# Kernel optimization log

Hardware: AMD Instinct MI355X
Metric: run time of the kernel (lower is better)

Reference implementation:

```python
import jax, jax.numpy as jnp
import numpy as np

IN_FEATURES = 512
HIDDEN = 512


def setup_inputs() -> dict:
    key = jax.random.key(0)
    ks = jax.random.split(key, 7)
    s = 1.0 / np.sqrt(IN_FEATURES)
    return {
        "x": jax.random.normal(ks[0], (8, 2048, IN_FEATURES), dtype=jnp.float32),
        "Wq": jax.random.uniform(ks[1], (IN_FEATURES, HIDDEN), jnp.float32, -s, s),
        "bq": jax.random.uniform(ks[2], (HIDDEN,), jnp.float32, -s, s),
        "Wk": jax.random.uniform(ks[3], (IN_FEATURES, HIDDEN), jnp.float32, -s, s),
        "bk": jax.random.uniform(ks[4], (HIDDEN,), jnp.float32, -s, s),
        "Wv": jax.random.uniform(ks[5], (IN_FEATURES, HIDDEN), jnp.float32, -s, s),
        "bv": jax.random.uniform(ks[6], (HIDDEN,), jnp.float32, -s, s),
    }


def reference(x, Wq, bq, Wk, bk, Wv, bv):
    # q,k,v: [b, s, h]
    q = jnp.einsum("bsf,fh->bsh", x, Wq) + bq
    k = jnp.einsum("bsf,fh->bsh", x, Wk) + bk
    v = jnp.einsum("bsf,fh->bsh", x, Wv) + bv
    # NOTE: no 1/sqrt(d) scaling, matching the original module.
    scores = jnp.einsum("bqh,bkh->bqk", q, k)  # [b, s, s]
    attn = jax.nn.softmax(scores, axis=-1)
    return jnp.einsum("bqk,bkh->bqh", attn, v)
```

## Files before the change

kernel.cpp:

```cpp
#include <hip/hip_runtime.h>
#include <hip/hip_fp16.h>


typedef _Float16 f16;
typedef __attribute__((ext_vector_type(8))) _Float16 f16x8;
typedef __attribute__((ext_vector_type(4))) _Float16 f16x4;
typedef __attribute__((ext_vector_type(4))) float f32x4;
typedef __attribute__((address_space(3))) char lds_t;

#define GADDR(p) ((const __attribute__((address_space(1))) void*)(p))
#define LADDR(p) ((__attribute__((address_space(3))) void*)(p))

__device__ __forceinline__ unsigned lds_u32(void* p) {
    return (unsigned)(unsigned long long)(lds_t*)p;
}

#define DSRD(dst, a) asm volatile("ds_read_b128 %0, %1" : "=v"(dst) : "v"(a))
#define WAITV0 asm volatile("s_waitcnt vmcnt(0)" ::: "memory")
#define WAITV4 asm volatile("s_waitcnt vmcnt(4)" ::: "memory")
#define WAITV8 asm volatile("s_waitcnt vmcnt(8)" ::: "memory")
#define WAITLG0 asm volatile("s_waitcnt lgkmcnt(0)" ::: "memory")

__device__ __forceinline__ void xcd_remap(int& bx, int& by, int& bz) {
    const int gx = gridDim.x, gy = gridDim.y;
    const int nwg = gx * gy * gridDim.z;
    const int f = (blockIdx.z * gy + blockIdx.y) * gx + blockIdx.x;
    int L = (f & 7) * (nwg >> 3) + (f >> 3);
    bx = L % gx; int r = L / gx; by = r % gy; bz = r / gy;
}

__global__ __launch_bounds__(256) void k_cvt(const float* __restrict__ x,
                                             f16* __restrict__ xh,
                                             const float* __restrict__ Wq,
                                             const float* __restrict__ Wk,
                                             const float* __restrict__ Wv,
                                             f16* __restrict__ Wt) {
    int bid = blockIdx.x;
    if (bid < 8192) {
        long i = (long)bid * 256 + threadIdx.x;
        float4 v = ((const float4*)x)[i];
        f16x4 h = { (f16)v.x, (f16)v.y, (f16)v.z, (f16)v.w };
        ((f16x4*)xh)[i] = h;
    } else {
        int id = (bid - 8192) * 256 + threadIdx.x;
        int w = id >> 18, rem = id & 262143;
        int kk = rem >> 9, n = rem & 511;
        const float* W = (w == 0) ? Wq : (w == 1) ? Wk : Wv;
        Wt[((long)w << 18) + ((long)n << 9) + kk] = (f16)W[((long)kk << 9) + n];
    }
}

#define G128STAGE(BUF, K0)                                                                  \
  { _Pragma("unroll") for (int i_ = 0; i_ < 4; ++i_) {                                      \
      const f16* sa_ = A + (rowA0 + i_ * 32 + (tid >> 3)) * (long)K + (K0) + colSw;         \
      __builtin_amdgcn_global_load_lds(GADDR(sa_),                                          \
          LADDR(smem + (BUF) * 32768 + i_ * 4096 + wave * 1024), 16, 0, 0);                 \
      const f16* sb_ = Bt + (rowB0 + i_ * 32 + (tid >> 3)) * (long)K + (K0) + colSw;        \
      __builtin_amdgcn_global_load_lds(GADDR(sb_),                                          \
          LADDR(smem + (BUF) * 32768 + 16384 + i_ * 4096 + wave * 1024), 16, 0, 0);         \
    } }

template <int MODE, int NT>
__global__ __launch_bounds__(256) void k_g128(const f16* __restrict__ Ain,
                                              const f16* __restrict__ Btin,
                                              void* __restrict__ Cv,
                                              void* __restrict__ CvAlt,
                                              const float* __restrict__ b0,
                                              const float* __restrict__ b1,
                                              const float* __restrict__ b2,
                                              int N,
                                              long sA, long sB, long sC) {
    constexpr int K = NT << 6;

    int bxi, byi, bz;
    xcd_remap(bxi, byi, bz);
    const f16* A  = Ain  + bz * sA;
    const f16* Bt = Btin + bz * sB;
    __shared__ __align__(16) char smem[65536];
    const unsigned sbase = lds_u32(smem);

    const int tid = threadIdx.x;
    const int wave = tid >> 6, lane = tid & 63;
    const int l15 = lane & 15, l4 = lane >> 4;
    const int wm = (wave >> 1) * 64, wn = (wave & 1) * 64;
    const long rowA0 = (long)byi * 128;
    const long rowB0 = (long)bxi * 128;

    const unsigned sw = (unsigned)((l15 & 7) << 4);
    const unsigned cb0 = (unsigned)(l4 * 16) ^ sw;
    const unsigned cb1 = (unsigned)(64 + l4 * 16) ^ sw;
    const int colSw = (((tid & 7) ^ ((tid >> 3) & 7)) << 3);

    f32x4 acc[4][4] = {};

    G128STAGE(0, 0);
    int cur = 0;
#pragma unroll 1
    for (int t = 0; t < NT; ++t) {
        if (t + 1 < NT) { G128STAGE(cur ^ 1, (t + 1) << 6); WAITV8; }
        else            { WAITV0; }
        __builtin_amdgcn_s_barrier();

        f16x8 af[4][2], bf[4][2];
        const unsigned aB = sbase + (unsigned)cur * 32768u;
        const unsigned bB = aB + 16384u;
#pragma unroll
        for (int mi = 0; mi < 4; ++mi) {
            unsigned ra = wm + mi * 16 + l15;
            DSRD(af[mi][0], aB + ra * 128 + cb0);
            DSRD(af[mi][1], aB + ra * 128 + cb1);
        }
#pragma unroll
        for (int nj = 0; nj < 4; ++nj) {
            unsigned rb = wn + nj * 16 + l15;
            DSRD(bf[nj][0], bB + rb * 128 + cb0);
            DSRD(bf[nj][1], bB + rb * 128 + cb1);
        }
        WAITLG0;
        __builtin_amdgcn_sched_barrier(0);
        __builtin_amdgcn_s_setprio(1);
#pragma unroll
        for (int mi = 0; mi < 4; ++mi)
#pragma unroll
            for (int nj = 0; nj < 4; ++nj)
#pragma unroll
                for (int ks = 0; ks < 2; ++ks)
                    acc[mi][nj] = __builtin_amdgcn_mfma_f32_16x16x32_f16(
                        af[mi][ks], bf[nj][ks], acc[mi][nj], 0, 0, 0);
        __builtin_amdgcn_s_setprio(0);
        __builtin_amdgcn_s_barrier();
        cur ^= 1;
    }

    if constexpr (MODE == 0) {
        float* C = (float*)Cv + bz * sC;
#pragma unroll
        for (int mi = 0; mi < 4; ++mi)
#pragma unroll
            for (int nj = 0; nj < 4; ++nj) {
                long gr = rowA0 + wm + mi * 16 + l4 * 4;
                int  gc = (int)rowB0 + wn + nj * 16 + l15;
#pragma unroll
                for (int r = 0; r < 4; ++r)
                    C[(gr + r) * (long)N + gc] = acc[mi][nj][r];
            }
    } else {
        if (bz == 2) {
            f16* VT = (f16*)CvAlt;
#pragma unroll
            for (int mi = 0; mi < 4; ++mi)
#pragma unroll
                for (int nj = 0; nj < 4; ++nj) {
                    long gr = rowA0 + wm + mi * 16 + l4 * 4;
                    int  gc = (int)rowB0 + wn + nj * 16 + l15;
                    float bv_ = b2[gc];
                    long b = gr >> 11, sL = gr & 2047;
                    f16x4 o = { (f16)(acc[mi][nj][0] + bv_),
                                (f16)(acc[mi][nj][1] + bv_),
                                (f16)(acc[mi][nj][2] + bv_),
                                (f16)(acc[mi][nj][3] + bv_) };
                    *(f16x4*)(VT + (b << 20) + ((long)gc << 11) + sL) = o;
                }
        } else {
            const float* bias = (bz == 0) ? b0 : b1;
            f16* C = (f16*)Cv + bz * sC;
#pragma unroll
            for (int mi = 0; mi < 4; ++mi)
#pragma unroll
                for (int nj = 0; nj < 4; ++nj) {
                    long gr = rowA0 + wm + mi * 16 + l4 * 4;
                    int  gc = (int)rowB0 + wn + nj * 16 + l15;
                    float bv_ = bias[gc];
#pragma unroll
                    for (int r = 0; r < 4; ++r)
                        C[(gr + r) * (long)N + gc] = (f16)(acc[mi][nj][r] + bv_);
                }
        }
    }
}

#define S512STAGE(BUF, K0)                                                                  \
  { _Pragma("unroll") for (int i_ = 0; i_ < 2; ++i_) {                                      \
      const f16* sa_ = A + (rowA0 + i_ * 64 + (tid >> 3)) * 512L + (K0) + colSw;            \
      __builtin_amdgcn_global_load_lds(GADDR(sa_),                                          \
          LADDR(smem + (BUF) * 32768 + i_ * 8192 + wid * 1024), 16, 0, 0);                  \
      const f16* sb_ = Bt + (rowB0 + i_ * 64 + (tid >> 3)) * 512L + (K0) + colSw;           \
      __builtin_amdgcn_global_load_lds(GADDR(sb_),                                          \
          LADDR(smem + (BUF) * 32768 + 16384 + i_ * 8192 + wid * 1024), 16, 0, 0);          \
    } }

__global__ __launch_bounds__(512) void k_scores512(const f16* __restrict__ Ain,
                                                   const f16* __restrict__ Btin,
                                                   f16* __restrict__ Cv) {
    constexpr int NT = 8;
    int bxi, byi, bz;
    xcd_remap(bxi, byi, bz);
    const f16* A  = Ain  + (long)bz * 2048 * 512;
    const f16* Bt = Btin + (long)bz * 2048 * 512;
    __shared__ __align__(16) char smem[65536];
    const unsigned sbase = lds_u32(smem);

    const int tid = threadIdx.x;
    const int wid = tid >> 6, lane = tid & 63;
    const int l15 = lane & 15, l4 = lane >> 4;
    const int wm = (wid >> 2) * 64, wn = (wid & 3) * 32;
    const long rowA0 = (long)byi * 128;
    const long rowB0 = (long)bxi * 128;

    const unsigned sw = (unsigned)((l15 & 7) << 4);
    const unsigned cb0 = (unsigned)(l4 * 16) ^ sw;
    const unsigned cb1 = (unsigned)(64 + l4 * 16) ^ sw;
    const int colSw = (((tid & 7) ^ ((tid >> 3) & 7)) << 3);

    f32x4 acc[4][2] = {};

    S512STAGE(0, 0);
    int cur = 0;
#pragma unroll 1
    for (int t = 0; t < NT; ++t) {
        if (t + 1 < NT) { S512STAGE(cur ^ 1, (t + 1) << 6); WAITV4; }
        else            { WAITV0; }
        __builtin_amdgcn_s_barrier();

        f16x8 af[4][2], bf[2][2];
        const unsigned aB = sbase + (unsigned)cur * 32768u;
        const unsigned bB = aB + 16384u;
#pragma unroll
        for (int mi = 0; mi < 4; ++mi) {
            unsigned ra = wm + mi * 16 + l15;
            DSRD(af[mi][0], aB + ra * 128 + cb0);
            DSRD(af[mi][1], aB + ra * 128 + cb1);
        }
#pragma unroll
        for (int nj = 0; nj < 2; ++nj) {
            unsigned rb = wn + nj * 16 + l15;
            DSRD(bf[nj][0], bB + rb * 128 + cb0);
            DSRD(bf[nj][1], bB + rb * 128 + cb1);
        }
        WAITLG0;
        __builtin_amdgcn_sched_barrier(0);
        __builtin_amdgcn_s_setprio(1);
#pragma unroll
        for (int mi = 0; mi < 4; ++mi)
#pragma unroll
            for (int nj = 0; nj < 2; ++nj)
#pragma unroll
                for (int ks = 0; ks < 2; ++ks)
                    acc[mi][nj] = __builtin_amdgcn_mfma_f32_16x16x32_f16(
                        af[mi][ks], bf[nj][ks], acc[mi][nj], 0, 0, 0);
        __builtin_amdgcn_s_setprio(0);
        __builtin_amdgcn_s_barrier();
        cur ^= 1;
    }

    f16* C = Cv + (long)bz * 2048 * 2048;
#pragma unroll
    for (int mi = 0; mi < 4; ++mi)
#pragma unroll
        for (int nj = 0; nj < 2; ++nj) {
            long gr = rowA0 + wm + mi * 16 + l4 * 4;
            int  gc = (int)rowB0 + wn + nj * 16 + l15;
#pragma unroll
            for (int r = 0; r < 4; ++r)
                C[(gr + r) * 2048L + gc] = (f16)acc[mi][nj][r];
        }
}

__global__ __launch_bounds__(256) void k_softmax(f16* __restrict__ P) {
    const long row = blockIdx.x;
    f16* p = P + row * 2048;
    const int tid = threadIdx.x, lane = tid & 63, wave = tid >> 6;

    f16x8 v = ((const f16x8*)p)[tid];
    float f[8];
#pragma unroll
    for (int j = 0; j < 8; ++j) f[j] = (float)v[j];
    float m = fmaxf(fmaxf(fmaxf(f[0], f[1]), fmaxf(f[2], f[3])),
                    fmaxf(fmaxf(f[4], f[5]), fmaxf(f[6], f[7])));
#pragma unroll
    for (int off = 32; off; off >>= 1) m = fmaxf(m, __shfl_xor(m, off));

    __shared__ float red[4];
    __shared__ float bc[2];
    if (lane == 0) red[wave] = m;
    __syncthreads();
    if (tid == 0) bc[0] = fmaxf(fmaxf(red[0], red[1]), fmaxf(red[2], red[3]));
    __syncthreads();
    m = bc[0];

    float e[8], sum = 0.f;
#pragma unroll
    for (int j = 0; j < 8; ++j) { e[j] = __expf(f[j] - m); sum += e[j]; }
#pragma unroll
    for (int off = 32; off; off >>= 1) sum += __shfl_xor(sum, off);
    if (lane == 0) red[wave] = sum;
    __syncthreads();
    if (tid == 0) bc[1] = (red[0] + red[1]) + (red[2] + red[3]);
    __syncthreads();
    float inv = 1.f / bc[1];

    f16x8 o;
#pragma unroll
    for (int j = 0; j < 8; ++j) o[j] = (f16)(e[j] * inv);
    ((f16x8*)p)[tid] = o;
}

extern "C" void kernel_launch(void* const* d_in, const int* in_sizes, int n_in,
                              void* d_out, int out_size, void* d_ws, size_t ws_size,
                              hipStream_t stream) {
    const float* x  = (const float*)d_in[0];
    const float* Wq = (const float*)d_in[1];
    const float* bq = (const float*)d_in[2];
    const float* Wk = (const float*)d_in[3];
    const float* bk = (const float*)d_in[4];
    const float* Wv = (const float*)d_in[5];
    const float* bv = (const float*)d_in[6];
    float* out = (float*)d_out;

    char* ws = (char*)d_ws;
    f16* vt = (f16*)(ws + 0);
    f16* xh = (f16*)(ws + 33554432);
    f16* Wt = (f16*)(ws + 50331648);
    f16* P8 = (f16*)(ws + 33554432);
    f16* qh = (f16*)d_out;
    f16* kh = (f16*)((char*)d_out + 16777216);

    k_cvt<<<11264, 256, 0, stream>>>(x, xh, Wq, Wk, Wv, Wt);

    k_g128<1, 8><<<dim3(4, 128, 3), 256, 0, stream>>>(
        xh, Wt, qh, vt, bq, bk, bv, 512,
        0, (long)512 * 512, (long)16384 * 512);

    k_scores512<<<dim3(16, 16, 8), 512, 0, stream>>>(qh, kh, P8);

    k_softmax<<<16384, 256, 0, stream>>>(P8);

    k_g128<0, 32><<<dim3(4, 16, 8), 256, 0, stream>>>(
        P8, vt, out, nullptr, nullptr, nullptr, nullptr, 512,
        (long)2048 * 2048, (long)512 * 2048, (long)2048 * 512);
}
```

Baseline: 154.2 us.

## Use K=32 tiles with half the LDS for projection and scores GEMMs

```diff
diff --git a/kernel.cpp b/kernel.cpp
--- a/kernel.cpp
+++ b/kernel.cpp
@@ -50,33 +50,34 @@
     }
 }
 
-#define G128STAGE(BUF, K0)                                                                  \
-  { _Pragma("unroll") for (int i_ = 0; i_ < 4; ++i_) {                                      \
-      const f16* sa_ = A + (rowA0 + i_ * 32 + (tid >> 3)) * (long)K + (K0) + colSw;         \
+
+#define B32STAGE(BUF, K0)                                                                   \
+  { _Pragma("unroll") for (int i_ = 0; i_ < 2; ++i_) {                                      \
+      const f16* sa_ = A + (rowA0 + i_ * 64 + (tid >> 2)) * (long)K + (K0) + colSw;         \
       __builtin_amdgcn_global_load_lds(GADDR(sa_),                                          \
-          LADDR(smem + (BUF) * 32768 + i_ * 4096 + wave * 1024), 16, 0, 0);                 \
-      const f16* sb_ = Bt + (rowB0 + i_ * 32 + (tid >> 3)) * (long)K + (K0) + colSw;        \
+          LADDR(smem + (BUF) * 16384 + i_ * 4096 + wave * 1024), 16, 0, 0);                 \
+      const f16* sb_ = Bt + (rowB0 + i_ * 64 + (tid >> 2)) * (long)K + (K0) + colSw;        \
       __builtin_amdgcn_global_load_lds(GADDR(sb_),                                          \
-          LADDR(smem + (BUF) * 32768 + 16384 + i_ * 4096 + wave * 1024), 16, 0, 0);         \
+          LADDR(smem + (BUF) * 16384 + 8192 + i_ * 4096 + wave * 1024), 16, 0, 0);          \
     } }
 
 template <int MODE, int NT>
-__global__ __launch_bounds__(256) void k_g128(const f16* __restrict__ Ain,
-                                              const f16* __restrict__ Btin,
-                                              void* __restrict__ Cv,
-                                              void* __restrict__ CvAlt,
-                                              const float* __restrict__ b0,
-                                              const float* __restrict__ b1,
-                                              const float* __restrict__ b2,
-                                              int N,
-                                              long sA, long sB, long sC) {
-    constexpr int K = NT << 6;
+__global__ __launch_bounds__(256) void k_b32(const f16* __restrict__ Ain,
+                                             const f16* __restrict__ Btin,
+                                             void* __restrict__ Cv,
+                                             void* __restrict__ CvAlt,
+                                             const float* __restrict__ b0,
+                                             const float* __restrict__ b1,
+                                             const float* __restrict__ b2,
+                                             int N,
+                                             long sA, long sB, long sC) {
+    constexpr int K = NT << 5;
 
     int bxi, byi, bz;
     xcd_remap(bxi, byi, bz);
     const f16* A  = Ain  + bz * sA;
     const f16* Bt = Btin + bz * sB;
-    __shared__ __align__(16) char smem[65536];
+    __shared__ __align__(16) char smem[32768];
     const unsigned sbase = lds_u32(smem);
 
     const int tid = threadIdx.x;
@@ -86,36 +87,29 @@
     const long rowA0 = (long)byi * 128;
     const long rowB0 = (long)bxi * 128;
 
-    const unsigned sw = (unsigned)((l15 & 7) << 4);
-    const unsigned cb0 = (unsigned)(l4 * 16) ^ sw;
-    const unsigned cb1 = (unsigned)(64 + l4 * 16) ^ sw;
-    const int colSw = (((tid & 7) ^ ((tid >> 3) & 7)) << 3);
+    const unsigned sw = (unsigned)(((l15 & 3) ^ ((l15 >> 2) & 3)) << 4);
+    const unsigned cb = (unsigned)(l4 * 16) ^ sw;
+    const int colSw = (((tid & 3) ^ ((tid >> 2) & 3) ^ ((tid >> 4) & 3)) << 3);
 
     f32x4 acc[4][4] = {};
 
-    G128STAGE(0, 0);
+    B32STAGE(0, 0);
     int cur = 0;
 #pragma unroll 1
     for (int t = 0; t < NT; ++t) {
-        if (t + 1 < NT) { G128STAGE(cur ^ 1, (t + 1) << 6); WAITV8; }
+        if (t + 1 < NT) { B32STAGE(cur ^ 1, (t + 1) << 5); WAITV4; }
         else            { WAITV0; }
         __builtin_amdgcn_s_barrier();
 
-        f16x8 af[4][2], bf[4][2];
-        const unsigned aB = sbase + (unsigned)cur * 32768u;
-        const unsigned bB = aB + 16384u;
-#pragma unroll
-        for (int mi = 0; mi < 4; ++mi) {
-            unsigned ra = wm + mi * 16 + l15;
-            DSRD(af[mi][0], aB + ra * 128 + cb0);
-            DSRD(af[mi][1], aB + ra * 128 + cb1);
-        }
-#pragma unroll
-        for (int nj = 0; nj < 4; ++nj) {
-            unsigned rb = wn + nj * 16 + l15;
-            DSRD(bf[nj][0], bB + rb * 128 + cb0);
-            DSRD(bf[nj][1], bB + rb * 128 + cb1);
-        }
+        f16x8 af[4], bf[4];
+        const unsigned aB = sbase + (unsigned)cur * 16384u;
+        const unsigned bB = aB + 8192u;
+#pragma unroll
+        for (int mi = 0; mi < 4; ++mi)
+            DSRD(af[mi], aB + (wm + mi * 16 + l15) * 64 + cb);
+#pragma unroll
+        for (int nj = 0; nj < 4; ++nj)
+            DSRD(bf[nj], bB + (wn + nj * 16 + l15) * 64 + cb);
         WAITLG0;
         __builtin_amdgcn_sched_barrier(0);
         __builtin_amdgcn_s_setprio(1);
@@ -123,28 +117,14 @@
         for (int mi = 0; mi < 4; ++mi)
 #pragma unroll
             for (int nj = 0; nj < 4; ++nj)
-#pragma unroll
-                for (int ks = 0; ks < 2; ++ks)
-                    acc[mi][nj] = __builtin_amdgcn_mfma_f32_16x16x32_f16(
-                        af[mi][ks], bf[nj][ks], acc[mi][nj], 0, 0, 0);
+                acc[mi][nj] = __builtin_amdgcn_mfma_f32_16x16x32_f16(
+                    af[mi], bf[nj], acc[mi][nj], 0, 0, 0);
         __builtin_amdgcn_s_setprio(0);
         __builtin_amdgcn_s_barrier();
         cur ^= 1;
     }
 
-    if constexpr (MODE == 0) {
-        float* C = (float*)Cv + bz * sC;
-#pragma unroll
-        for (int mi = 0; mi < 4; ++mi)
-#pragma unroll
-            for (int nj = 0; nj < 4; ++nj) {
-                long gr = rowA0 + wm + mi * 16 + l4 * 4;
-                int  gc = (int)rowB0 + wn + nj * 16 + l15;
-#pragma unroll
-                for (int r = 0; r < 4; ++r)
-                    C[(gr + r) * (long)N + gc] = acc[mi][nj][r];
-            }
-    } else {
+    if constexpr (MODE == 1) {
         if (bz == 2) {
             f16* VT = (f16*)CvAlt;
 #pragma unroll
@@ -176,34 +156,49 @@
                         C[(gr + r) * (long)N + gc] = (f16)(acc[mi][nj][r] + bv_);
                 }
         }
+    } else {
+        f16* C = (f16*)Cv + bz * sC;
+#pragma unroll
+        for (int mi = 0; mi < 4; ++mi)
+#pragma unroll
+            for (int nj = 0; nj < 4; ++nj) {
+                long gr = rowA0 + wm + mi * 16 + l4 * 4;
+                int  gc = (int)rowB0 + wn + nj * 16 + l15;
+#pragma unroll
+                for (int r = 0; r < 4; ++r)
+                    C[(gr + r) * (long)N + gc] = (f16)acc[mi][nj][r];
+            }
     }
 }
 
-#define S512STAGE(BUF, K0)                                                                  \
-  { _Pragma("unroll") for (int i_ = 0; i_ < 2; ++i_) {                                      \
-      const f16* sa_ = A + (rowA0 + i_ * 64 + (tid >> 3)) * 512L + (K0) + colSw;            \
+#define G128STAGE(BUF, K0)                                                                  \
+  { _Pragma("unroll") for (int i_ = 0; i_ < 4; ++i_) {                                      \
+      const f16* sa_ = A + (rowA0 + i_ * 32 + (tid >> 3)) * (long)K + (K0) + colSw;         \
       __builtin_amdgcn_global_load_lds(GADDR(sa_),                                          \
-          LADDR(smem + (BUF) * 32768 + i_ * 8192 + wid * 1024), 16, 0, 0);                  \
-      const f16* sb_ = Bt + (rowB0 + i_ * 64 + (tid >> 3)) * 512L + (K0) + colSw;           \
+          LADDR(smem + (BUF) * 32768 + i_ * 4096 + wave * 1024), 16, 0, 0);                 \
+      const f16* sb_ = Bt + (rowB0 + i_ * 32 + (tid >> 3)) * (long)K + (K0) + colSw;        \
       __builtin_amdgcn_global_load_lds(GADDR(sb_),                                          \
-          LADDR(smem + (BUF) * 32768 + 16384 + i_ * 8192 + wid * 1024), 16, 0, 0);          \
+          LADDR(smem + (BUF) * 32768 + 16384 + i_ * 4096 + wave * 1024), 16, 0, 0);         \
     } }
 
-__global__ __launch_bounds__(512) void k_scores512(const f16* __restrict__ Ain,
-                                                   const f16* __restrict__ Btin,
-                                                   f16* __restrict__ Cv) {
-    constexpr int NT = 8;
+template <int NT>
+__global__ __launch_bounds__(256) void k_g128(const f16* __restrict__ Ain,
+                                              const f16* __restrict__ Btin,
+                                              float* __restrict__ Cout,
+                                              int N, long sA, long sB, long sC) {
+    constexpr int K = NT << 6;
+
     int bxi, byi, bz;
     xcd_remap(bxi, byi, bz);
-    const f16* A  = Ain  + (long)bz * 2048 * 512;
-    const f16* Bt = Btin + (long)bz * 2048 * 512;
+    const f16* A  = Ain  + bz * sA;
+    const f16* Bt = Btin + bz * sB;
     __shared__ __align__(16) char smem[65536];
     const unsigned sbase = lds_u32(smem);
 
     const int tid = threadIdx.x;
-    const int wid = tid >> 6, lane = tid & 63;
+    const int wave = tid >> 6, lane = tid & 63;
     const int l15 = lane & 15, l4 = lane >> 4;
-    const int wm = (wid >> 2) * 64, wn = (wid & 3) * 32;
+    const int wm = (wave >> 1) * 64, wn = (wave & 1) * 64;
     const long rowA0 = (long)byi * 128;
     const long rowB0 = (long)bxi * 128;
 
@@ -212,17 +207,17 @@
     const unsigned cb1 = (unsigned)(64 + l4 * 16) ^ sw;
     const int colSw = (((tid & 7) ^ ((tid >> 3) & 7)) << 3);
 
-    f32x4 acc[4][2] = {};
-
-    S512STAGE(0, 0);
+    f32x4 acc[4][4] = {};
+
+    G128STAGE(0, 0);
     int cur = 0;
 #pragma unroll 1
     for (int t = 0; t < NT; ++t) {
-        if (t + 1 < NT) { S512STAGE(cur ^ 1, (t + 1) << 6); WAITV4; }
+        if (t + 1 < NT) { G128STAGE(cur ^ 1, (t + 1) << 6); WAITV8; }
         else            { WAITV0; }
         __builtin_amdgcn_s_barrier();
 
-        f16x8 af[4][2], bf[2][2];
+        f16x8 af[4][2], bf[4][2];
         const unsigned aB = sbase + (unsigned)cur * 32768u;
         const unsigned bB = aB + 16384u;
 #pragma unroll
@@ -232,7 +227,7 @@
             DSRD(af[mi][1], aB + ra * 128 + cb1);
         }
 #pragma unroll
-        for (int nj = 0; nj < 2; ++nj) {
+        for (int nj = 0; nj < 4; ++nj) {
             unsigned rb = wn + nj * 16 + l15;
             DSRD(bf[nj][0], bB + rb * 128 + cb0);
             DSRD(bf[nj][1], bB + rb * 128 + cb1);
@@ -243,7 +238,7 @@
 #pragma unroll
         for (int mi = 0; mi < 4; ++mi)
 #pragma unroll
-            for (int nj = 0; nj < 2; ++nj)
+            for (int nj = 0; nj < 4; ++nj)
 #pragma unroll
                 for (int ks = 0; ks < 2; ++ks)
                     acc[mi][nj] = __builtin_amdgcn_mfma_f32_16x16x32_f16(
@@ -253,16 +248,16 @@
         cur ^= 1;
     }
 
-    f16* C = Cv + (long)bz * 2048 * 2048;
+    float* C = Cout + bz * sC;
 #pragma unroll
     for (int mi = 0; mi < 4; ++mi)
 #pragma unroll
-        for (int nj = 0; nj < 2; ++nj) {
+        for (int nj = 0; nj < 4; ++nj) {
             long gr = rowA0 + wm + mi * 16 + l4 * 4;
             int  gc = (int)rowB0 + wn + nj * 16 + l15;
 #pragma unroll
             for (int r = 0; r < 4; ++r)
-                C[(gr + r) * 2048L + gc] = (f16)acc[mi][nj][r];
+                C[(gr + r) * (long)N + gc] = acc[mi][nj][r];
         }
 }
 
@@ -327,15 +322,17 @@
 
     k_cvt<<<11264, 256, 0, stream>>>(x, xh, Wq, Wk, Wv, Wt);
 
-    k_g128<1, 8><<<dim3(4, 128, 3), 256, 0, stream>>>(
+    k_b32<1, 16><<<dim3(4, 128, 3), 256, 0, stream>>>(
         xh, Wt, qh, vt, bq, bk, bv, 512,
         0, (long)512 * 512, (long)16384 * 512);
 
-    k_scores512<<<dim3(16, 16, 8), 512, 0, stream>>>(qh, kh, P8);
+    k_b32<2, 16><<<dim3(16, 16, 8), 256, 0, stream>>>(
+        qh, kh, P8, nullptr, nullptr, nullptr, nullptr, 2048,
+        (long)2048 * 512, (long)2048 * 512, (long)2048 * 2048);
 
     k_softmax<<<16384, 256, 0, stream>>>(P8);
 
-    k_g128<0, 32><<<dim3(4, 16, 8), 256, 0, stream>>>(
-        P8, vt, out, nullptr, nullptr, nullptr, nullptr, 512,
+    k_g128<32><<<dim3(4, 16, 8), 256, 0, stream>>>(
+        P8, vt, out, 512,
         (long)2048 * 2048, (long)512 * 2048, (long)2048 * 512);
 }
```

After: 162.8 us. 1.06x slower.

## Chain four column tiles per scores block to overlap epilogue stores with loads

Applied to the files above, without the earlier changes.

```diff
diff --git a/kernel.cpp b/kernel.cpp
--- a/kernel.cpp
+++ b/kernel.cpp
@@ -19,6 +19,7 @@
 #define WAITV0 asm volatile("s_waitcnt vmcnt(0)" ::: "memory")
 #define WAITV4 asm volatile("s_waitcnt vmcnt(4)" ::: "memory")
 #define WAITV8 asm volatile("s_waitcnt vmcnt(8)" ::: "memory")
+#define WAITV36 asm volatile("s_waitcnt vmcnt(36)" ::: "memory")
 #define WAITLG0 asm volatile("s_waitcnt lgkmcnt(0)" ::: "memory")
 
 __device__ __forceinline__ void xcd_remap(int& bx, int& by, int& bz) {
@@ -179,12 +180,12 @@
     }
 }
 
-#define S512STAGE(BUF, K0)                                                                  \
+#define S512STAGE(BUF, RB, K0)                                                              \
   { _Pragma("unroll") for (int i_ = 0; i_ < 2; ++i_) {                                      \
       const f16* sa_ = A + (rowA0 + i_ * 64 + (tid >> 3)) * 512L + (K0) + colSw;            \
       __builtin_amdgcn_global_load_lds(GADDR(sa_),                                          \
           LADDR(smem + (BUF) * 32768 + i_ * 8192 + wid * 1024), 16, 0, 0);                  \
-      const f16* sb_ = Bt + (rowB0 + i_ * 64 + (tid >> 3)) * 512L + (K0) + colSw;           \
+      const f16* sb_ = Bt + ((RB) + i_ * 64 + (tid >> 3)) * 512L + (K0) + colSw;            \
       __builtin_amdgcn_global_load_lds(GADDR(sb_),                                          \
           LADDR(smem + (BUF) * 32768 + 16384 + i_ * 8192 + wid * 1024), 16, 0, 0);          \
     } }
@@ -192,7 +193,6 @@
 __global__ __launch_bounds__(512) void k_scores512(const f16* __restrict__ Ain,
                                                    const f16* __restrict__ Btin,
                                                    f16* __restrict__ Cv) {
-    constexpr int NT = 8;
     int bxi, byi, bz;
     xcd_remap(bxi, byi, bz);
     const f16* A  = Ain  + (long)bz * 2048 * 512;
@@ -205,21 +205,28 @@
     const int l15 = lane & 15, l4 = lane >> 4;
     const int wm = (wid >> 2) * 64, wn = (wid & 3) * 32;
     const long rowA0 = (long)byi * 128;
-    const long rowB0 = (long)bxi * 128;
+    const long chain0 = (long)bxi * 4;
 
     const unsigned sw = (unsigned)((l15 & 7) << 4);
     const unsigned cb0 = (unsigned)(l4 * 16) ^ sw;
     const unsigned cb1 = (unsigned)(64 + l4 * 16) ^ sw;
     const int colSw = (((tid & 7) ^ ((tid >> 3) & 7)) << 3);
 
+    f16* C = Cv + (long)bz * 2048 * 2048;
     f32x4 acc[4][2] = {};
 
-    S512STAGE(0, 0);
+    S512STAGE(0, chain0 * 128, 0);
     int cur = 0;
 #pragma unroll 1
-    for (int t = 0; t < NT; ++t) {
-        if (t + 1 < NT) { S512STAGE(cur ^ 1, (t + 1) << 6); WAITV4; }
-        else            { WAITV0; }
+    for (int u = 0; u < 32; ++u) {
+        if (u + 1 < 32) {
+            const int un = u + 1;
+            S512STAGE(cur ^ 1, (chain0 + (un >> 3)) * 128, (un & 7) << 6);
+            if ((u & 7) == 0 && u) { WAITV36; }
+            else                   { WAITV4;  }
+        } else {
+            WAITV0;
+        }
         __builtin_amdgcn_s_barrier();
 
         f16x8 af[4][2], bf[2][2];
@@ -251,19 +258,29 @@
         __builtin_amdgcn_s_setprio(0);
         __builtin_amdgcn_s_barrier();
         cur ^= 1;
+
+        if ((u & 7) == 7) {
+            const long rowB0c = (chain0 + (u >> 3)) * 128;
+#pragma unroll
+            for (int mi = 0; mi < 4; ++mi)
+#pragma unroll
+                for (int nj = 0; nj < 2; ++nj) {
+                    long gr = rowA0 + wm + mi * 16 + l4 * 4;
+                    int  gc = (int)rowB0c + wn + nj * 16 + l15;
+#pragma unroll
+                    for (int r = 0; r < 4; ++r)
+                        C[(gr + r) * 2048L + gc] = (f16)acc[mi][nj][r];
+                }
+            asm volatile("" ::: "memory");
+            if (u != 31) {
+#pragma unroll
+                for (int mi = 0; mi < 4; ++mi)
+#pragma unroll
+                    for (int nj = 0; nj < 2; ++nj)
+                        acc[mi][nj] = (f32x4){0.f, 0.f, 0.f, 0.f};
+            }
+        }
     }
-
-    f16* C = Cv + (long)bz * 2048 * 2048;
-#pragma unroll
-    for (int mi = 0; mi < 4; ++mi)
-#pragma unroll
-        for (int nj = 0; nj < 2; ++nj) {
-            long gr = rowA0 + wm + mi * 16 + l4 * 4;
-            int  gc = (int)rowB0 + wn + nj * 16 + l15;
-#pragma unroll
-            for (int r = 0; r < 4; ++r)
-                C[(gr + r) * 2048L + gc] = (f16)acc[mi][nj][r];
-        }
 }
 
 __global__ __launch_bounds__(256) void k_softmax(f16* __restrict__ P) {
@@ -331,7 +348,7 @@
         xh, Wt, qh, vt, bq, bk, bv, 512,
         0, (long)512 * 512, (long)16384 * 512);
 
-    k_scores512<<<dim3(16, 16, 8), 512, 0, stream>>>(qh, kh, P8);
+    k_scores512<<<dim3(4, 16, 8), 512, 0, stream>>>(qh, kh, P8);
 
     k_softmax<<<16384, 256, 0, stream>>>(P8);
 
```

Result: slower. 162.5 us (+5.4%).
